# Optimization experiments

Measured on AMD Instinct MI355X. Metric: run time of the kernel, lower is better.

The kernel has to match this reference:

```python
import jax, jax.numpy as jnp
import numpy as np

WIN = 20  # patch_project window_size
HID = 128


def _lstm_layer(x, w_ih, w_hh, b_ih, b_hh):
    """x: [B,T,D] -> (outputs [B,T,H], final h [B,H]). PyTorch gate order i,f,g,o."""
    B = x.shape[0]
    H = w_hh.shape[1]
    # precompute input contribution for all timesteps: [B,T,4H]
    x_pre = jnp.einsum('btd,gd->btg', x, w_ih) + b_ih + b_hh

    def step(carry, xp):
        h, c = carry
        gates = xp + h @ w_hh.T  # [B,4H]
        i, f, g, o = jnp.split(gates, 4, axis=-1)
        i = jax.nn.sigmoid(i)
        f = jax.nn.sigmoid(f)
        g = jnp.tanh(g)
        o = jax.nn.sigmoid(o)
        c = f * c + i * g
        h = o * jnp.tanh(c)
        return (h, c), h

    h0 = jnp.zeros((B, H), x.dtype)
    c0 = jnp.zeros((B, H), x.dtype)
    (h_f, _), ys = jax.lax.scan(step, (h0, c0), x_pre.transpose(1, 0, 2))
    return ys.transpose(1, 0, 2), h_f


def setup_inputs() -> dict:
    key = jax.random.key(0)
    ks = jax.random.split(key, 20)
    B, S, C = 64, 2048, 32
    D_in = WIN * C          # 640
    D_p = D_in // 2         # 320
    H = HID
    label_len = 48
    s = 0.02
    inp = {
        'inputs': jax.random.normal(ks[0], (B, S, C), jnp.float32),
        '_x': jnp.zeros((B, 4), jnp.float32),
        'y': jnp.zeros((B, label_len), jnp.float32),
        '_y': jnp.zeros((B, 4), jnp.float32),
        'proj_w': jax.random.normal(ks[1], (D_p, D_in), jnp.float32) * s,
        'proj_b': jax.random.normal(ks[2], (D_p,), jnp.float32) * s,
        'w_ih0': jax.random.normal(ks[3], (4 * H, D_p), jnp.float32) * s,
        'w_hh0': jax.random.normal(ks[4], (4 * H, H), jnp.float32) * s,
        'b_ih0': jax.random.normal(ks[5], (4 * H,), jnp.float32) * s,
        'b_hh0': jax.random.normal(ks[6], (4 * H,), jnp.float32) * s,
        'w_ih_rest': jax.random.normal(ks[7], (3, 4 * H, H), jnp.float32) * s,
        'w_hh_rest': jax.random.normal(ks[8], (3, 4 * H, H), jnp.float32) * s,
        'b_ih_rest': jax.random.normal(ks[9], (3, 4 * H), jnp.float32) * s,
        'b_hh_rest': jax.random.normal(ks[10], (3, 4 * H), jnp.float32) * s,
        'out_w': jax.random.normal(ks[11], (label_len, H), jnp.float32) * s,
        'out_b': jax.random.normal(ks[12], (label_len,), jnp.float32) * s,
    }
    return inp


def reference(inputs, _x, y, _y, proj_w, proj_b, w_ih0, w_hh0, b_ih0, b_hh0,
              w_ih_rest, w_hh_rest, b_ih_rest, b_hh_rest, out_w, out_b):
    B, S, C = inputs.shape
    L_out = S - WIN
    idx = jnp.arange(L_out)[:, None] + jnp.arange(WIN)[None, :]
    windows = inputs[:, idx, :].reshape(B, L_out, WIN * C)
    # projection1 (dropout is inference no-op)
    x = jnp.einsum('btd,pd->btp', windows, proj_w) + proj_b
    # 4-layer LSTM (dropout between layers is inference no-op)
    x, h = _lstm_layer(x, w_ih0, w_hh0, b_ih0, b_hh0)
    for l in range(3):
        x, h = _lstm_layer(x, w_ih_rest[l], w_hh_rest[l], b_ih_rest[l], b_hh_rest[l])
    # final hidden state of last layer -> [B,1,H] -> output layer -> [B,1,label_len]
    out = h[:, None, :] @ out_w.T + out_b
    return out
```

## Files before the change

### kernel.cpp

```cpp
#include <hip/hip_runtime.h>
#include <stdint.h>
#include <stddef.h>

typedef __bf16 bf16_t;
typedef bf16_t bf16x8 __attribute__((ext_vector_type(8)));
typedef bf16_t bf16x4 __attribute__((ext_vector_type(4)));
typedef float  f32x4  __attribute__((ext_vector_type(4)));

#define T_STEPS 2028
#define SEQ     2048
#define CIN     32
#define NG      32
#define MB      2
#define CH      32
#define NCH     64
#define RING    4

#define OFF_EFFW   0u
#define OFF_BIAS   655360u
#define OFF_WHH    663552u
#define OFF_WIH    1187840u
#define OFF_HFIN   1581056u
#define OFF_CNT    1613824u
#define OFF_XRING  1638400u
#define OFF_YRING  35192832u

__device__ __forceinline__ int endk(int k) {
  int e = (k + 1) * CH;
  return e > T_STEPS ? T_STEPS : e;
}

__device__ __forceinline__ void spin_ge(uint32_t* p, uint32_t tgt) {
  while (atomicAdd(p, 0u) < tgt) __builtin_amdgcn_s_sleep(2);
}
__device__ __forceinline__ void publish(uint32_t* p, uint32_t v) {
  __builtin_amdgcn_fence(__ATOMIC_RELEASE, "agent");
  atomicMax(p, v);
}

__device__ __forceinline__ float fsigm(float x) {
  return __builtin_amdgcn_rcpf(1.0f + __builtin_amdgcn_exp2f(x * -1.44269504089f));
}
__device__ __forceinline__ float ftanh(float x) {
  return 1.0f - 2.0f * __builtin_amdgcn_rcpf(1.0f + __builtin_amdgcn_exp2f(x * 2.88539008178f));
}

__device__ __forceinline__ bf16x8 ldg8(const bf16_t* p) { return *(const bf16x8*)p; }
__device__ __forceinline__ bf16x4 ldg4(const bf16_t* p) { return *(const bf16x4*)p; }

__device__ __forceinline__ bf16x8 ldg_cvt8(const float* p) {
  const f32x4 a = *(const f32x4*)p;
  const f32x4 b = *(const f32x4*)(p + 4);
  bf16x8 r;
  r[0] = (bf16_t)a[0]; r[1] = (bf16_t)a[1]; r[2] = (bf16_t)a[2]; r[3] = (bf16_t)a[3];
  r[4] = (bf16_t)b[0]; r[5] = (bf16_t)b[1]; r[6] = (bf16_t)b[2]; r[7] = (bf16_t)b[3];
  return r;
}


__global__ void k_prep_misc(const float* __restrict__ w_hh0,
                            const float* __restrict__ w_ih_rest,
                            const float* __restrict__ w_hh_rest,
                            const float* __restrict__ b_ih_rest,
                            const float* __restrict__ b_hh_rest,
                            uint8_t* __restrict__ ws) {
  const int bid = blockIdx.x;
  const int l = bid >> 9;
  const int p = bid & 511;
  const int orig = (p & 3) * 128 + (p >> 2);
  const int tid = threadIdx.x;
  bf16_t* whh = (bf16_t*)(ws + OFF_WHH);
  bf16_t* wih = (bf16_t*)(ws + OFF_WIH);
  float* bias = (float*)(ws + OFF_BIAS);
  const float* src = (l == 0) ? (w_hh0 + orig * 128)
                              : (w_hh_rest + ((size_t)(l - 1) * 512 + orig) * 128);
  whh[((size_t)l * 512 + p) * 128 + tid] = (bf16_t)src[tid];
  if (l < 3)
    wih[((size_t)l * 512 + p) * 128 + tid] = (bf16_t)w_ih_rest[((size_t)l * 512 + orig) * 128 + tid];
  if (l >= 1 && tid == 0)
    bias[l * 512 + p] = b_ih_rest[(l - 1) * 512 + orig] + b_hh_rest[(l - 1) * 512 + orig];
  if (bid == 0) {
    uint32_t* cnt = (uint32_t*)(ws + OFF_CNT);
    for (int i = tid; i < 12 * 32 * 16; i += 128) cnt[i] = 0;
  }
}

__global__ void k_prep_effw(const float* __restrict__ proj_w,
                            const float* __restrict__ proj_b,
                            const float* __restrict__ w_ih0,
                            const float* __restrict__ b_ih0,
                            const float* __restrict__ b_hh0,
                            uint8_t* __restrict__ ws) {
  __shared__ float wr[320];
  const int p = blockIdx.x;
  const int orig = (p & 3) * 128 + (p >> 2);
  const int tid = threadIdx.x;
  for (int i = tid; i < 320; i += 256) wr[i] = w_ih0[(size_t)orig * 320 + i];
  __syncthreads();
  bf16_t* effw = (bf16_t*)(ws + OFF_EFFW);
  for (int kk = tid; kk < 640; kk += 256) {
    float a = 0.f;
    for (int z = 0; z < 320; ++z) a += wr[z] * proj_w[(size_t)z * 640 + kk];
    effw[(size_t)p * 640 + kk] = (bf16_t)a;
  }
  if (tid == 0) {
    float a = 0.f;
    for (int z = 0; z < 320; ++z) a += wr[z] * proj_b[z];
    ((float*)(ws + OFF_BIAS))[p] = a + b_ih0[orig] + b_hh0[orig];
  }
}

__global__ __launch_bounds__(256, 1) void k_pipeline(const float* __restrict__ in,
                                                     uint8_t* __restrict__ ws) {
  __shared__ __align__(16) bf16_t h_lds[2][16][136];
  __shared__ f32x4 gate_buf[4][2][32];

  const int s = blockIdx.x >> 5;
  const int g = blockIdx.x & 31;
  const int tid = threadIdx.x;
  const int lane = tid & 63;
  const int w = tid >> 6;
  const int q = lane >> 4;
  const int ln = lane & 15;

  uint32_t* cnt = (uint32_t*)(ws + OFF_CNT);
  bf16_t* xring = (bf16_t*)(ws + OFF_XRING);
  bf16_t* yring = (bf16_t*)(ws + OFF_YRING);

  if (s == 0) {
    const bf16_t* effw = (const bf16_t*)(ws + OFF_EFFW);
    uint32_t* my = cnt + (0 * NG + g) * 16;
    uint32_t* guard = cnt + (1 * NG + g) * 16;
    for (int k = 0; k < NCH; ++k) {
      if (tid == 0 && k >= RING) spin_ge(guard, (uint32_t)endk(k - RING));
      __syncthreads();
      const int t0 = k * CH;
      f32x4 acc[4][8];
#pragma unroll
      for (int mt = 0; mt < 4; ++mt)
#pragma unroll
        for (int nt = 0; nt < 8; ++nt) acc[mt][nt] = (f32x4){0.f, 0.f, 0.f, 0.f};
#pragma unroll
      for (int kt = 0; kt < 20; ++kt) {
        bf16x8 bfr[8];
#pragma unroll
        for (int nt = 0; nt < 8; ++nt)
          bfr[nt] = ldg8(effw + (size_t)((w * 8 + nt) * 16 + ln) * 640 + kt * 32 + q * 8);
#pragma unroll
        for (int mt = 0; mt < 4; ++mt) {
          int m = mt * 16 + ln;
          int trel = m >> 1, bb = m & 1;
          int tt = t0 + trel; if (tt > T_STEPS - 1) tt = T_STEPS - 1;
          bf16x8 afr = ldg_cvt8(in + (size_t)((g * MB + bb) * SEQ + tt + kt) * CIN + q * 8);
#pragma unroll
          for (int nt = 0; nt < 8; ++nt)
            acc[mt][nt] = __builtin_amdgcn_mfma_f32_16x16x32_bf16(afr, bfr[nt], acc[mt][nt], 0, 0, 0);
        }
      }
      bf16_t* xs = xring + (size_t)((0 * NG + g) * RING + (k & 3)) * (64 * 512);
#pragma unroll
      for (int mt = 0; mt < 4; ++mt)
#pragma unroll
        for (int nt = 0; nt < 8; ++nt)
#pragma unroll
          for (int r = 0; r < 4; ++r)
            xs[(size_t)(mt * 16 + q * 4 + r) * 512 + (w * 8 + nt) * 16 + ln] = (bf16_t)acc[mt][nt][r];
      __syncthreads();
      if (tid == 0) publish(my, (uint32_t)endk(k));
    }
  } else if (s <= 4) {
    const int l = s - 1;
    const bf16_t* whh = (const bf16_t*)(ws + OFF_WHH) + (size_t)l * 512 * 128;
    bf16x8 wfr[8][4];
#pragma unroll
    for (int mt = 0; mt < 8; ++mt)
#pragma unroll
      for (int kt = 0; kt < 4; ++kt)
        wfr[mt][kt] = ldg8(whh + (size_t)(w * 128 + mt * 16 + ln) * 128 + kt * 32 + q * 8);
    const int b_ep = lane >> 5;
    const int j_loc = lane & 31;
    const int jg = w * 32 + j_loc;
    f32x4 biasq = *(const f32x4*)((const float*)(ws + OFF_BIAS) + l * 512 + 4 * jg);
    float c = 0.f;
    {
      bf16_t* hz = &h_lds[0][0][0];
      for (int i = tid; i < 2 * 16 * 136; i += 256) hz[i] = (bf16_t)0.f;
    }
    __syncthreads();
    uint32_t* my = cnt + ((1 + l) * NG + g) * 16;
    uint32_t* prod = (l == 0) ? (cnt + (0 * NG + g) * 16) : (cnt + ((4 + l) * NG + g) * 16);
    uint32_t* yguard = cnt + ((5 + l) * NG + g) * 16;
    float* hfin = (float*)(ws + OFF_HFIN);
    const int ly = (l < 3) ? l : 0;

    for (int k = 0; k < NCH; ++k) {
      const int t0 = k * CH;
      const int tlen = (T_STEPS - t0 < CH) ? (T_STEPS - t0) : CH;
      if (tid == 0) {
        spin_ge(prod, (uint32_t)(t0 + tlen));
        if (l < 3 && k >= RING) spin_ge(yguard, (uint32_t)endk(k - RING));
        __builtin_amdgcn_fence(__ATOMIC_ACQUIRE, "agent");
      }
      __syncthreads();
      const bf16_t* xlane = xring + (size_t)((l * NG + g) * RING + (k & 3)) * (64 * 512)
                            + b_ep * 512 + 4 * jg;
      bf16_t* ylane = yring + (size_t)((ly * NG + g) * RING + (k & 3)) * (64 * 128)
                      + b_ep * 128 + jg;

      if (tlen == CH) {
        for (int half = 0; half < 2; ++half) {
          const int tb = t0 + half * 16;
          bf16x4 xq[16];
#pragma unroll
          for (int t = 0; t < 16; ++t) xq[t] = ldg4(xlane + (size_t)(half * 16 + t) * 1024);
          bf16_t yv[16];
#pragma unroll
          for (int t = 0; t < 16; ++t) {
            const int buf = (tb + t) & 1;
            f32x4 acc[8];
#pragma unroll
            for (int mt = 0; mt < 8; ++mt) acc[mt] = (f32x4){0.f, 0.f, 0.f, 0.f};
#pragma unroll
            for (int kt = 0; kt < 4; ++kt) {
              bf16x8 hk = *(const bf16x8*)&h_lds[buf][ln][kt * 32 + q * 8];
#pragma unroll
              for (int mt = 0; mt < 8; ++mt)
                acc[mt] = __builtin_amdgcn_mfma_f32_16x16x32_bf16(wfr[mt][kt], hk, acc[mt], 0, 0, 0);
            }
            if (ln < MB) {
#pragma unroll
              for (int mt = 0; mt < 8; ++mt)
                gate_buf[w][ln][mt * 4 + q] = acc[mt];
            }
            f32x4 gq = gate_buf[w][b_ep][j_loc];
            float gi = fsigm(gq[0] + (float)xq[t][0] + biasq[0]);
            float gf = fsigm(gq[1] + (float)xq[t][1] + biasq[1]);
            float gg = ftanh(gq[2] + (float)xq[t][2] + biasq[2]);
            float go = fsigm(gq[3] + (float)xq[t][3] + biasq[3]);
            c = gf * c + gi * gg;
            float hv = go * ftanh(c);
            h_lds[buf ^ 1][b_ep][jg] = (bf16_t)hv;
            yv[t] = (bf16_t)hv;
            asm volatile("s_waitcnt lgkmcnt(0)\n\ts_barrier" ::: "memory");
          }
          if (l < 3) {
#pragma unroll
            for (int t = 0; t < 16; ++t)
              ylane[(size_t)(half * 16 + t) * 256] = yv[t];
          }
        }
      } else {
        for (int trel = 0; trel < tlen; ++trel) {
          const int t = t0 + trel;
          const int buf = t & 1;
          bf16x4 xqs = ldg4(xlane + (size_t)trel * 1024);
          f32x4 acc[8];
#pragma unroll
          for (int mt = 0; mt < 8; ++mt) acc[mt] = (f32x4){0.f, 0.f, 0.f, 0.f};
#pragma unroll
          for (int kt = 0; kt < 4; ++kt) {
            bf16x8 hk = *(const bf16x8*)&h_lds[buf][ln][kt * 32 + q * 8];
#pragma unroll
            for (int mt = 0; mt < 8; ++mt)
              acc[mt] = __builtin_amdgcn_mfma_f32_16x16x32_bf16(wfr[mt][kt], hk, acc[mt], 0, 0, 0);
          }
          if (ln < MB) {
#pragma unroll
            for (int mt = 0; mt < 8; ++mt)
              gate_buf[w][ln][mt * 4 + q] = acc[mt];
          }
          f32x4 gq = gate_buf[w][b_ep][j_loc];
          float gi = fsigm(gq[0] + (float)xqs[0] + biasq[0]);
          float gf = fsigm(gq[1] + (float)xqs[1] + biasq[1]);
          float gg = ftanh(gq[2] + (float)xqs[2] + biasq[2]);
          float go = fsigm(gq[3] + (float)xqs[3] + biasq[3]);
          c = gf * c + gi * gg;
          float hv = go * ftanh(c);
          h_lds[buf ^ 1][b_ep][jg] = (bf16_t)hv;
          if (l < 3) ylane[(size_t)trel * 256] = (bf16_t)hv;
          if (l == 3 && t == T_STEPS - 1) hfin[(g * MB + b_ep) * 128 + jg] = hv;
          asm volatile("s_waitcnt lgkmcnt(0)\n\ts_barrier" ::: "memory");
        }
      }
      __syncthreads();
      if (tid == 0) publish(my, (uint32_t)(t0 + tlen));
    }
  } else {
    const int l = s - 4;
    const bf16_t* wih = (const bf16_t*)(ws + OFF_WIH) + (size_t)(l - 1) * 512 * 128;
    bf16x8 bfr[8][4];
#pragma unroll
    for (int nt = 0; nt < 8; ++nt)
#pragma unroll
      for (int kt = 0; kt < 4; ++kt)
        bfr[nt][kt] = ldg8(wih + (size_t)((w * 8 + nt) * 16 + ln) * 128 + kt * 32 + q * 8);
    uint32_t* my = cnt + ((4 + l) * NG + g) * 16;
    uint32_t* prod = cnt + (l * NG + g) * 16;
    uint32_t* xguard = cnt + ((1 + l) * NG + g) * 16;
    for (int k = 0; k < NCH; ++k) {
      if (tid == 0) {
        spin_ge(prod, (uint32_t)endk(k));
        if (k >= RING) spin_ge(xguard, (uint32_t)endk(k - RING));
        __builtin_amdgcn_fence(__ATOMIC_ACQUIRE, "agent");
      }
      __syncthreads();
      const bf16_t* ys = yring + (size_t)(((l - 1) * NG + g) * RING + (k & 3)) * (64 * 128);
      bf16_t* xs = xring + (size_t)((l * NG + g) * RING + (k & 3)) * (64 * 512);
      bf16x8 afr[4][4];
#pragma unroll
      for (int mt = 0; mt < 4; ++mt)
#pragma unroll
        for (int kt = 0; kt < 4; ++kt)
          afr[mt][kt] = ldg8(ys + (size_t)(mt * 16 + ln) * 128 + kt * 32 + q * 8);
#pragma unroll
      for (int mt = 0; mt < 4; ++mt) {
        f32x4 a8[8];
#pragma unroll
        for (int nt = 0; nt < 8; ++nt) a8[nt] = (f32x4){0.f, 0.f, 0.f, 0.f};
#pragma unroll
        for (int kt = 0; kt < 4; ++kt) {
#pragma unroll
          for (int nt = 0; nt < 8; ++nt)
            a8[nt] = __builtin_amdgcn_mfma_f32_16x16x32_bf16(afr[mt][kt], bfr[nt][kt], a8[nt], 0, 0, 0);
        }
#pragma unroll
        for (int nt = 0; nt < 8; ++nt)
#pragma unroll
          for (int r = 0; r < 4; ++r)
            xs[(size_t)(mt * 16 + q * 4 + r) * 512 + (w * 8 + nt) * 16 + ln] = (bf16_t)a8[nt][r];
      }
      __syncthreads();
      if (tid == 0) publish(my, (uint32_t)endk(k));
    }
  }
}

__global__ void k_out(const float* __restrict__ out_w,
                      const float* __restrict__ out_b,
                      const uint8_t* __restrict__ ws,
                      float* __restrict__ out) {
  const int idx = blockIdx.x * 256 + threadIdx.x;
  const int b = idx / 48, o = idx % 48;
  const float* h = (const float*)(ws + OFF_HFIN) + b * 128;
  const float* wrow = out_w + (size_t)o * 128;
  float a = out_b[o];
  for (int j = 0; j < 128; ++j) a += h[j] * wrow[j];
  out[idx] = a;
}

extern "C" void kernel_launch(void* const* d_in, const int* in_sizes, int n_in,
                              void* d_out, int out_size, void* d_ws, size_t ws_size,
                              hipStream_t stream) {
  (void)in_sizes; (void)n_in; (void)out_size; (void)ws_size;
  const float* inputs    = (const float*)d_in[0];
  const float* proj_w    = (const float*)d_in[4];
  const float* proj_b    = (const float*)d_in[5];
  const float* w_ih0     = (const float*)d_in[6];
  const float* w_hh0     = (const float*)d_in[7];
  const float* b_ih0     = (const float*)d_in[8];
  const float* b_hh0     = (const float*)d_in[9];
  const float* w_ih_rest = (const float*)d_in[10];
  const float* w_hh_rest = (const float*)d_in[11];
  const float* b_ih_rest = (const float*)d_in[12];
  const float* b_hh_rest = (const float*)d_in[13];
  const float* out_w     = (const float*)d_in[14];
  const float* out_b     = (const float*)d_in[15];
  uint8_t* ws = (uint8_t*)d_ws;
  float* out = (float*)d_out;

  k_prep_misc<<<dim3(2048), dim3(128), 0, stream>>>(w_hh0, w_ih_rest, w_hh_rest,
                                                    b_ih_rest, b_hh_rest, ws);
  k_prep_effw<<<dim3(512), dim3(256), 0, stream>>>(proj_w, proj_b, w_ih0, b_ih0, b_hh0, ws);
  k_pipeline<<<dim3(256), dim3(256), 0, stream>>>(inputs, ws);
  k_out<<<dim3(12), dim3(256), 0, stream>>>(out_w, out_b, ws, out);
}
```

Before: 2.735 ms.

## Replace per-step workgroup barrier in LSTM recurrence with LDS wave flags

Each of the four waves in a layer block now publishes its completed timestep in a shared-memory flag. Before each step it polls the other three waves' flags, with a short sleep, instead of every wave meeting at a workgroup barrier. The step body is moved into a lambda used by both the full-chunk path and the 12-step tail, which now also batches its y stores. The aim is to let waves drift slightly and avoid full barrier cost. The risks are polling and sleep latency, and correctness depending on volatile LDS ordering.

Measured after the change: 3.000 ms. +9.7%, slower.

```diff
diff --git a/kernel.cpp b/kernel.cpp
--- a/kernel.cpp
+++ b/kernel.cpp
@@ -114,6 +114,7 @@
                                                      uint8_t* __restrict__ ws) {
   __shared__ __align__(16) bf16_t h_lds[2][16][136];
   __shared__ f32x4 gate_buf[4][2][32];
+  __shared__ uint32_t hflag[32];
 
   const int s = blockIdx.x >> 5;
   const int g = blockIdx.x & 31;
@@ -185,6 +186,7 @@
     {
       bf16_t* hz = &h_lds[0][0][0];
       for (int i = tid; i < 2 * 16 * 136; i += 256) hz[i] = (bf16_t)0.f;
+      if (tid < 4) hflag[tid * 8] = 0;
     }
     __syncthreads();
     uint32_t* my = cnt + ((1 + l) * NG + g) * 16;
@@ -192,6 +194,46 @@
     uint32_t* yguard = cnt + ((5 + l) * NG + g) * 16;
     float* hfin = (float*)(ws + OFF_HFIN);
     const int ly = (l < 3) ? l : 0;
+    volatile uint32_t* vf = hflag;
+    const int f1 = ((w + 1) & 3) * 8, f2 = ((w + 2) & 3) * 8, f3 = ((w + 3) & 3) * 8;
+
+    auto do_step = [&](int t, bf16x4 xq, bf16_t& yv) {
+      const int buf = t & 1;
+      if (t > 0) {
+        const uint32_t tt = (uint32_t)t;
+        if (vf[f1] < tt || vf[f2] < tt || vf[f3] < tt) {
+          do { __builtin_amdgcn_s_sleep(1); } while (vf[f1] < tt || vf[f2] < tt || vf[f3] < tt);
+        }
+        asm volatile("" ::: "memory");
+      }
+      f32x4 acc[8];
+#pragma unroll
+      for (int mt = 0; mt < 8; ++mt) acc[mt] = (f32x4){0.f, 0.f, 0.f, 0.f};
+#pragma unroll
+      for (int kt = 0; kt < 4; ++kt) {
+        bf16x8 hk = *(const bf16x8*)&h_lds[buf][ln][kt * 32 + q * 8];
+#pragma unroll
+        for (int mt = 0; mt < 8; ++mt)
+          acc[mt] = __builtin_amdgcn_mfma_f32_16x16x32_bf16(wfr[mt][kt], hk, acc[mt], 0, 0, 0);
+      }
+      if (ln < MB) {
+#pragma unroll
+        for (int mt = 0; mt < 8; ++mt)
+          gate_buf[w][ln][mt * 4 + q] = acc[mt];
+      }
+      f32x4 gq = gate_buf[w][b_ep][j_loc];
+      float gi = fsigm(gq[0] + (float)xq[0] + biasq[0]);
+      float gf = fsigm(gq[1] + (float)xq[1] + biasq[1]);
+      float gg = ftanh(gq[2] + (float)xq[2] + biasq[2]);
+      float go = fsigm(gq[3] + (float)xq[3] + biasq[3]);
+      c = gf * c + gi * gg;
+      float hv = go * ftanh(c);
+      h_lds[buf ^ 1][b_ep][jg] = (bf16_t)hv;
+      yv = (bf16_t)hv;
+      if (l == 3 && t == T_STEPS - 1) hfin[(g * MB + b_ep) * 128 + jg] = hv;
+      asm volatile("s_waitcnt lgkmcnt(0)" ::: "memory");
+      if (lane == 0) vf[w * 8] = (uint32_t)(t + 1);
+    };
 
     for (int k = 0; k < NCH; ++k) {
       const int t0 = k * CH;
@@ -209,40 +251,12 @@
 
       if (tlen == CH) {
         for (int half = 0; half < 2; ++half) {
-          const int tb = t0 + half * 16;
           bf16x4 xq[16];
 #pragma unroll
           for (int t = 0; t < 16; ++t) xq[t] = ldg4(xlane + (size_t)(half * 16 + t) * 1024);
           bf16_t yv[16];
 #pragma unroll
-          for (int t = 0; t < 16; ++t) {
-            const int buf = (tb + t) & 1;
-            f32x4 acc[8];
-#pragma unroll
-            for (int mt = 0; mt < 8; ++mt) acc[mt] = (f32x4){0.f, 0.f, 0.f, 0.f};
-#pragma unroll
-            for (int kt = 0; kt < 4; ++kt) {
-              bf16x8 hk = *(const bf16x8*)&h_lds[buf][ln][kt * 32 + q * 8];
-#pragma unroll
-              for (int mt = 0; mt < 8; ++mt)
-                acc[mt] = __builtin_amdgcn_mfma_f32_16x16x32_bf16(wfr[mt][kt], hk, acc[mt], 0, 0, 0);
-            }
-            if (ln < MB) {
-#pragma unroll
-              for (int mt = 0; mt < 8; ++mt)
-                gate_buf[w][ln][mt * 4 + q] = acc[mt];
-            }
-            f32x4 gq = gate_buf[w][b_ep][j_loc];
-            float gi = fsigm(gq[0] + (float)xq[t][0] + biasq[0]);
-            float gf = fsigm(gq[1] + (float)xq[t][1] + biasq[1]);
-            float gg = ftanh(gq[2] + (float)xq[t][2] + biasq[2]);
-            float go = fsigm(gq[3] + (float)xq[t][3] + biasq[3]);
-            c = gf * c + gi * gg;
-            float hv = go * ftanh(c);
-            h_lds[buf ^ 1][b_ep][jg] = (bf16_t)hv;
-            yv[t] = (bf16_t)hv;
-            asm volatile("s_waitcnt lgkmcnt(0)\n\ts_barrier" ::: "memory");
-          }
+          for (int t = 0; t < 16; ++t) do_step(t0 + half * 16 + t, xq[t], yv[t]);
           if (l < 3) {
 #pragma unroll
             for (int t = 0; t < 16; ++t)
@@ -250,36 +264,16 @@
           }
         }
       } else {
-        for (int trel = 0; trel < tlen; ++trel) {
-          const int t = t0 + trel;
-          const int buf = t & 1;
-          bf16x4 xqs = ldg4(xlane + (size_t)trel * 1024);
-          f32x4 acc[8];
-#pragma unroll
-          for (int mt = 0; mt < 8; ++mt) acc[mt] = (f32x4){0.f, 0.f, 0.f, 0.f};
-#pragma unroll
-          for (int kt = 0; kt < 4; ++kt) {
-            bf16x8 hk = *(const bf16x8*)&h_lds[buf][ln][kt * 32 + q * 8];
-#pragma unroll
-            for (int mt = 0; mt < 8; ++mt)
-              acc[mt] = __builtin_amdgcn_mfma_f32_16x16x32_bf16(wfr[mt][kt], hk, acc[mt], 0, 0, 0);
-          }
-          if (ln < MB) {
-#pragma unroll
-            for (int mt = 0; mt < 8; ++mt)
-              gate_buf[w][ln][mt * 4 + q] = acc[mt];
-          }
-          f32x4 gq = gate_buf[w][b_ep][j_loc];
-          float gi = fsigm(gq[0] + (float)xqs[0] + biasq[0]);
-          float gf = fsigm(gq[1] + (float)xqs[1] + biasq[1]);
-          float gg = ftanh(gq[2] + (float)xqs[2] + biasq[2]);
-          float go = fsigm(gq[3] + (float)xqs[3] + biasq[3]);
-          c = gf * c + gi * gg;
-          float hv = go * ftanh(c);
-          h_lds[buf ^ 1][b_ep][jg] = (bf16_t)hv;
-          if (l < 3) ylane[(size_t)trel * 256] = (bf16_t)hv;
-          if (l == 3 && t == T_STEPS - 1) hfin[(g * MB + b_ep) * 128 + jg] = hv;
-          asm volatile("s_waitcnt lgkmcnt(0)\n\ts_barrier" ::: "memory");
+        bf16x4 xq[12];
+#pragma unroll
+        for (int t = 0; t < 12; ++t) xq[t] = ldg4(xlane + (size_t)t * 1024);
+        bf16_t yv[12];
+#pragma unroll
+        for (int t = 0; t < 12; ++t) do_step(t0 + t, xq[t], yv[t]);
+        if (l < 3) {
+#pragma unroll
+          for (int t = 0; t < 12; ++t)
+            ylane[(size_t)t * 256] = yv[t];
         }
       }
       __syncthreads();
```
